# Optimization experiments

Hardware: AMD Instinct MI355X
Metric: run time of the kernel (lower is better)

Reference implementation:

```python
import jax, jax.numpy as jnp
import numpy as np

BN_EPS = 1e-5


def setup_inputs() -> dict:
    key = jax.random.key(0)
    k1, k2, k3, k4 = jax.random.split(key, 4)
    B, H, W, C = 2, 256, 256, 256
    x = jax.random.normal(k1, (B, H, W, C), dtype=jnp.float32)
    # 1x1 conv weights (bias=False), randomly initialized each forward in the original
    w_down = jax.random.normal(k2, (16, C), dtype=jnp.float32) * (1.0 / np.sqrt(C))
    w_up = jax.random.normal(k3, (C, 16), dtype=jnp.float32) * (1.0 / np.sqrt(16))
    w_final = jax.random.normal(k4, (C, 2 * C), dtype=jnp.float32) * (1.0 / np.sqrt(2 * C))
    return {"x": x, "w_down": w_down, "w_up": w_up, "w_final": w_final}


def reference(x, w_down, w_up, w_final):
    # x: [B, H, W, C] -> NCHW
    x = jnp.transpose(x, (0, 3, 1, 2))  # [B, C, H, W]
    B, C, H, W = x.shape
    # fresh BatchNorm2d in training mode: batch stats, weight=1, bias=0
    mean = jnp.mean(x, axis=(0, 2, 3), keepdims=True)
    var = jnp.var(x, axis=(0, 2, 3), keepdims=True)  # biased variance
    xn = (x - mean) * jax.lax.rsqrt(var + BN_EPS)  # [B, C, H, W]
    # relu -> sigmoid
    a = jax.nn.sigmoid(jax.nn.relu(xn))
    # down-channel 1x1 conv: C -> 16
    y = jnp.einsum('oc,bchw->bohw', w_down, a)  # [B, 16, H, W]
    f = y.reshape(B, 16, H * W)  # flattened per-sample [16, HW]
    # channel self-attention; NOTE: source bug reuses Gram of sample 0 for sample 1
    G0 = f[0] @ f[0].T  # [16, 16]
    out0 = G0 @ f[0]    # [16, HW]
    out1 = G0 @ f[1]    # [16, HW]  (faithful to xcam4b = Dot(xcam3a, xcam1b))
    xcam4 = jnp.stack([out0, out1], axis=0).reshape(B, 16, H, W)
    # up-channel 1x1 conv: 16 -> C
    up = jnp.einsum('co,bohw->bchw', w_up, xcam4)  # [B, C, H, W]
    cat = jnp.concatenate([xn, up], axis=1)  # [B, 2C, H, W]
    # final down-channel 1x1 conv: 2C -> C
    out = jnp.einsum('oc,bchw->bohw', w_final, cat)  # [B, C, H, W]
    return out
```

## Files before the change

kernel.cpp:

```cpp
#include <hip/hip_runtime.h>
#include <stdint.h>

typedef __attribute__((ext_vector_type(8))) short bf16x8;
typedef __attribute__((ext_vector_type(4))) float f32x4;

#define CC 256
#define HWP 65536

__device__ __forceinline__ unsigned short f2bf(float f) {
    union { float f; unsigned int u; } v; v.f = f;
    unsigned int u = v.u;
    return (unsigned short)((u + 0x7fffu + ((u >> 16) & 1u)) >> 16);
}
__device__ __forceinline__ unsigned int f2bf2(float lo, float hi) {
    return (unsigned)f2bf(lo) | ((unsigned)f2bf(hi) << 16);
}
__device__ __forceinline__ float sigm_relu(float xn) {
    float xr = fmaxf(xn, 0.f);
    float e = __expf(-xr);
    return __builtin_amdgcn_rcpf(1.f + e);
}

__global__ __launch_bounds__(512, 8) void k1_part(const float* __restrict__ x,
                                                  float* __restrict__ part) {
    __shared__ float red[8][520];
    const int t = threadIdx.x, bid = blockIdx.x;
    const int c4 = (t & 63) * 4, po = t >> 6;
    const float* xp = x + ((size_t)(bid * 256 + po)) * CC + c4;
    f32x4 s = {0.f, 0.f, 0.f, 0.f}, q = {0.f, 0.f, 0.f, 0.f};
    #pragma unroll 8
    for (int p = 0; p < 32; ++p) {
        f32x4 v = *(const f32x4*)(xp + (size_t)p * 8 * CC);
        s += v; q += v * v;
    }
    *(f32x4*)&red[po][c4] = s;
    *(f32x4*)&red[po][256 + c4] = q;
    __syncthreads();
    float r = 0.f;
    #pragma unroll
    for (int po2 = 0; po2 < 8; ++po2) r += red[po2][t];
    part[bid * 512 + t] = r;
}

__global__ __launch_bounds__(256) void k2a_red(const float* __restrict__ part,
                                               float* __restrict__ p2) {
    int t = threadIdx.x, r = blockIdx.x;
    float s = 0.f, q = 0.f;
    #pragma unroll
    for (int i = 0; i < 16; ++i) {
        s += part[(size_t)(r * 16 + i) * 512 + t];
        q += part[(size_t)(r * 16 + i) * 512 + 256 + t];
    }
    p2[r * 512 + t] = s;
    p2[r * 512 + 256 + t] = q;
}

__global__ __launch_bounds__(256) void k2b_stats(const float* __restrict__ p2,
                                                 float* __restrict__ mg,
                                                 float* __restrict__ ig) {
    int c = threadIdx.x;
    float s = 0.f, q = 0.f;
    #pragma unroll
    for (int r = 0; r < 32; ++r) { s += p2[r * 512 + c]; q += p2[r * 512 + 256 + c]; }
    float mean = s * (1.f / 131072.f);
    float var  = q * (1.f / 131072.f) - mean * mean;
    mg[c] = mean;
    ig[c] = rsqrtf(var + 1e-5f);
}

__global__ __launch_bounds__(512) void k3_gram(const float* __restrict__ x,
                                               const float* __restrict__ wd,
                                               const float* __restrict__ mg,
                                               const float* __restrict__ ig,
                                               float* __restrict__ gpart) {
    __shared__ uint4 apack[2048];
    __shared__ float y_s[2][16][68];
    const int t = threadIdx.x;
    const int w = t >> 6, lm = t & 15, lk = (t >> 4) & 3;
    const int h = w & 1, ntile = w >> 1;
    uint4 wfrag[4];
    #pragma unroll
    for (int kt = 0; kt < 4; ++kt) {
        const int kbr = h * 16 + kt * 4 + lk;
        f32x4 wa = *(const f32x4*)(wd + lm * 256 + kbr * 8);
        f32x4 wb = *(const f32x4*)(wd + lm * 256 + kbr * 8 + 4);
        wfrag[kt] = (uint4){f2bf2(wa[0], wa[1]), f2bf2(wa[2], wa[3]),
                            f2bf2(wb[0], wb[1]), f2bf2(wb[2], wb[3])};
    }
    const int kb = t & 31, c0 = kb * 8, nb = t >> 5;
    f32x4 m0 = *(const f32x4*)(mg + c0), m1 = *(const f32x4*)(mg + c0 + 4);
    f32x4 i0 = *(const f32x4*)(ig + c0), i1 = *(const f32x4*)(ig + c0 + 4);
    const float mm[8] = {m0[0],m0[1],m0[2],m0[3],m1[0],m1[1],m1[2],m1[3]};
    const float ii[8] = {i0[0],i0[1],i0[2],i0[3],i1[0],i1[1],i1[2],i1[3]};
    const int o1 = t >> 4, o2 = t & 15;
    float g = 0.f;
    for (int st = 0; st < 4; ++st) {
        const float* xb = x + ((size_t)(blockIdx.x * 256 + st * 64 + nb)) * CC + c0;
        #pragma unroll
        for (int rep = 0; rep < 4; ++rep) {
            int n = rep * 16 + nb;
            const float* xp = xb + (size_t)rep * 16 * CC;
            f32x4 v0 = *(const f32x4*)xp;
            f32x4 v1 = *(const f32x4*)(xp + 4);
            float vv[8] = {v0[0],v0[1],v0[2],v0[3],v1[0],v1[1],v1[2],v1[3]};
            unsigned aw[4];
            #pragma unroll
            for (int hh = 0; hh < 4; ++hh) {
                float a0 = sigm_relu((vv[2*hh]   - mm[2*hh])   * ii[2*hh]);
                float a1 = sigm_relu((vv[2*hh+1] - mm[2*hh+1]) * ii[2*hh+1]);
                aw[hh] = f2bf2(a0, a1);
            }
            apack[kb * 64 + (n ^ kb)] = (uint4){aw[0], aw[1], aw[2], aw[3]};
        }
        __syncthreads();
        f32x4 accY = {0.f, 0.f, 0.f, 0.f};
        #pragma unroll
        for (int kt = 0; kt < 4; ++kt) {
            const int kbr = h * 16 + kt * 4 + lk;
            uint4 u = apack[kbr * 64 + ((ntile * 16 + lm) ^ kbr)];
            accY = __builtin_amdgcn_mfma_f32_16x16x32_bf16(*(bf16x8*)&wfrag[kt], *(bf16x8*)&u, accY, 0, 0, 0);
        }
        #pragma unroll
        for (int i = 0; i < 4; ++i) y_s[h][lk * 4 + i][ntile * 16 + lm] = accY[i];
        __syncthreads();
        if (t < 256) {
            #pragma unroll
            for (int p4 = 0; p4 < 16; ++p4) {
                f32x4 a0 = *(const f32x4*)&y_s[0][o1][p4 * 4];
                f32x4 a1 = *(const f32x4*)&y_s[1][o1][p4 * 4];
                f32x4 b0 = *(const f32x4*)&y_s[0][o2][p4 * 4];
                f32x4 b1 = *(const f32x4*)&y_s[1][o2][p4 * 4];
                f32x4 ya = a0 + a1, yb = b0 + b1;
                g += ya[0]*yb[0] + ya[1]*yb[1] + ya[2]*yb[2] + ya[3]*yb[3];
            }
        }
        __syncthreads();
    }
    if (t < 256) gpart[blockIdx.x * 256 + t] = g;
}

__global__ __launch_bounds__(256) void k4_R(const float* __restrict__ gpart,
                                            const float* __restrict__ wd,
                                            float* __restrict__ Rg) {
    __shared__ float G_s[256];
    const int t = threadIdx.x;
    float g = 0.f;
    #pragma unroll 8
    for (int i = 0; i < 256; ++i) g += gpart[i * 256 + t];
    G_s[t] = g;
    __syncthreads();
    #pragma unroll
    for (int o = 0; o < 16; ++o) {
        float r = 0.f;
        #pragma unroll
        for (int o2 = 0; o2 < 16; ++o2) r += G_s[o * 16 + o2] * wd[o2 * 256 + t];
        Rg[o * 256 + t] = r;
    }
}

__global__ __launch_bounds__(256) void k5_wcb(const float* __restrict__ wf,
                                              const float* __restrict__ wu,
                                              const float* __restrict__ Rg,
                                              unsigned short* __restrict__ wcb) {
    __shared__ float M_s[16][17];
    const int t = threadIdx.x;
    const int lr = t >> 4, j = t & 15;
    const int r = blockIdx.x * 16 + lr;
    const float* wfr = wf + (size_t)r * 512;
    float m = 0.f;
    for (int c = 0; c < 256; ++c) m += wfr[256 + c] * wu[c * 16 + j];
    M_s[lr][j] = m;
    __syncthreads();
    float Ml[16];
    #pragma unroll
    for (int o = 0; o < 16; ++o) Ml[o] = M_s[lr][o];
    unsigned short* wrow = wcb + (size_t)r * 512;
    for (int i = 0; i < 16; ++i) {
        int c = j + 16 * i;
        wrow[c] = f2bf(wfr[c]);
        float kv = 0.f;
        #pragma unroll
        for (int o = 0; o < 16; ++o) kv += Ml[o] * Rg[o * 256 + c];
        wrow[256 + c] = f2bf(kv);
    }
}

__global__ __launch_bounds__(512, 4) void k6_main(const float* __restrict__ x,
                                                  const unsigned short* __restrict__ wcb,
                                                  const float* __restrict__ mg,
                                                  const float* __restrict__ ig,
                                                  float* __restrict__ out) {
    __shared__ __align__(16) char smem[69632];
    uint4* zpack = (uint4*)smem;
    float* T = (float*)smem;
    const int t = threadIdx.x;
    const int tile = blockIdx.x;
    const int b = tile >> 10;
    const int pw = (tile & 1023) * 64;
    {
        const int kb = t & 31, c0 = kb * 8, nb = t >> 5;
        f32x4 m0 = *(const f32x4*)(mg + c0), m1 = *(const f32x4*)(mg + c0 + 4);
        f32x4 i0 = *(const f32x4*)(ig + c0), i1 = *(const f32x4*)(ig + c0 + 4);
        float mm[8] = {m0[0],m0[1],m0[2],m0[3],m1[0],m1[1],m1[2],m1[3]};
        float ii[8] = {i0[0],i0[1],i0[2],i0[3],i1[0],i1[1],i1[2],i1[3]};
        const float* xb = x + ((size_t)(b * HWP + pw + nb)) * CC + c0;
        #pragma unroll
        for (int rep = 0; rep < 4; ++rep) {
            int n = rep * 16 + nb;
            const float* xp = xb + (size_t)rep * 16 * CC;
            f32x4 v0 = *(const f32x4*)xp;
            f32x4 v1 = *(const f32x4*)(xp + 4);
            float vv[8] = {v0[0],v0[1],v0[2],v0[3],v1[0],v1[1],v1[2],v1[3]};
            unsigned xw[4], aw[4];
            #pragma unroll
            for (int hh = 0; hh < 4; ++hh) {
                float xn0 = (vv[2*hh]   - mm[2*hh])   * ii[2*hh];
                float xn1 = (vv[2*hh+1] - mm[2*hh+1]) * ii[2*hh+1];
                xw[hh] = f2bf2(xn0, xn1);
                aw[hh] = f2bf2(sigm_relu(xn0), sigm_relu(xn1));
            }
            zpack[kb * 64 + (n ^ kb)] = (uint4){xw[0], xw[1], xw[2], xw[3]};
            zpack[(kb + 32) * 64 + (n ^ (kb + 32))] = (uint4){aw[0], aw[1], aw[2], aw[3]};
        }
    }
    __syncthreads();
    const int w = t >> 6, lm = t & 15, lk = (t >> 4) & 3;
    const unsigned short* wrow = wcb + (size_t)(w * 32 + lm) * 512 + lk * 8;
    f32x4 acc[4][2];
    #pragma unroll
    for (int mt = 0; mt < 4; ++mt)
        #pragma unroll
        for (int nt = 0; nt < 2; ++nt) acc[mt][nt] = (f32x4){0.f, 0.f, 0.f, 0.f};
    #pragma unroll 4
    for (int kt = 0; kt < 16; ++kt) {
        const int kbr = kt * 4 + lk;
        bf16x8 zfr[4], wfr[2];
        #pragma unroll
        for (int mt = 0; mt < 4; ++mt) {
            uint4 u = zpack[kbr * 64 + ((mt * 16 + lm) ^ kbr)];
            zfr[mt] = *(bf16x8*)&u;
        }
        #pragma unroll
        for (int nt = 0; nt < 2; ++nt)
            wfr[nt] = *(const bf16x8*)(wrow + (size_t)nt * 16 * 512 + kt * 32);
        #pragma unroll
        for (int mt = 0; mt < 4; ++mt)
            #pragma unroll
            for (int nt = 0; nt < 2; ++nt)
                acc[mt][nt] = __builtin_amdgcn_mfma_f32_16x16x32_bf16(zfr[mt], wfr[nt], acc[mt][nt], 0, 0, 0);
    }
    __syncthreads();
    #pragma unroll
    for (int nt = 0; nt < 2; ++nt) {
        const int ch = w * 32 + nt * 16 + lm;
        #pragma unroll
        for (int mt = 0; mt < 4; ++mt)
            *(f32x4*)&T[ch * 68 + mt * 16 + lk * 4] = acc[mt][nt];
    }
    __syncthreads();
    {
        const int row0 = t >> 4, pxq = t & 15;
        float* ob = out + (size_t)b * 256 * HWP + pw + pxq * 4;
        #pragma unroll
        for (int j = 0; j < 8; ++j) {
            const int row = j * 32 + row0;
            f32x4 v = *(const f32x4*)&T[row * 68 + pxq * 4];
            __builtin_nontemporal_store(v, (f32x4*)(ob + (size_t)row * HWP));
        }
    }
}

extern "C" void kernel_launch(void* const* d_in, const int* in_sizes, int n_in,
                              void* d_out, int out_size, void* d_ws, size_t ws_size,
                              hipStream_t stream) {
    const float* x  = (const float*)d_in[0];
    const float* wd = (const float*)d_in[1];
    const float* wu = (const float*)d_in[2];
    const float* wf = (const float*)d_in[3];
    float* out = (float*)d_out;
    char* ws = (char*)d_ws;
    unsigned short* wcb = (unsigned short*)ws;
    float* part  = (float*)(ws + 262144);
    float* p2    = (float*)(ws + 1310720);
    float* mg    = (float*)(ws + 1376256);
    float* ig    = (float*)(ws + 1377280);
    float* gpart = (float*)(ws + 1378304);
    float* Rg    = (float*)(ws + 1640448);

    k1_part <<<dim3(512),  dim3(512), 0, stream>>>(x, part);
    k2a_red <<<dim3(32),   dim3(256), 0, stream>>>(part, p2);
    k2b_stats<<<dim3(1),   dim3(256), 0, stream>>>(p2, mg, ig);
    k3_gram <<<dim3(256),  dim3(512), 0, stream>>>(x, wd, mg, ig, gpart);
    k4_R    <<<dim3(1),    dim3(256), 0, stream>>>(gpart, wd, Rg);
    k5_wcb  <<<dim3(16),   dim3(256), 0, stream>>>(wf, wu, Rg, wcb);
    k6_main <<<dim3(2048), dim3(512), 0, stream>>>(x, wcb, mg, ig, out);
}
```

Before: 175.8 us.

## Make k6_main persistent with register-prefetched tiles and direct MFMA output stores

The main GEMM kernel becomes a persistent-style kernel of 1024 threads, each block processing 8 pixel tiles. The next tile's input is prefetched into registers while the current tile runs its MFMAs. The shared-memory transpose of the output is dropped: each wave now owns 16 output channels and stores accumulators directly to global memory with nontemporal stores. The intent is to hide global load latency and cut LDS round trips, at the cost of fewer blocks (256), extra barriers, and narrower 64-byte output segments per row. Bf16 packing also switches to the library conversion routine.

```diff
diff --git a/kernel.cpp b/kernel.cpp
--- a/kernel.cpp
+++ b/kernel.cpp
@@ -1,5 +1,7 @@
 #include <hip/hip_runtime.h>
+#include <hip/hip_bf16.h>
 #include <stdint.h>
+#include <string.h>
 
 typedef __attribute__((ext_vector_type(8))) short bf16x8;
 typedef __attribute__((ext_vector_type(4))) float f32x4;
@@ -14,6 +16,12 @@
 }
 __device__ __forceinline__ unsigned int f2bf2(float lo, float hi) {
     return (unsigned)f2bf(lo) | ((unsigned)f2bf(hi) << 16);
+}
+__device__ __forceinline__ unsigned int pk2(float lo, float hi) {
+    union { __hip_bfloat16 b; unsigned short s; } ul, uh;
+    ul.b = __float2bfloat16(lo);
+    uh.b = __float2bfloat16(hi);
+    return (unsigned)ul.s | ((unsigned)uh.s << 16);
 }
 __device__ __forceinline__ float sigm_relu(float xn) {
     float xr = fmaxf(xn, 0.f);
@@ -185,89 +193,95 @@
     }
 }
 
-__global__ __launch_bounds__(512, 4) void k6_main(const float* __restrict__ x,
-                                                  const unsigned short* __restrict__ wcb,
-                                                  const float* __restrict__ mg,
-                                                  const float* __restrict__ ig,
-                                                  float* __restrict__ out) {
-    __shared__ __align__(16) char smem[69632];
-    uint4* zpack = (uint4*)smem;
-    float* T = (float*)smem;
+__global__ __launch_bounds__(1024, 4) void k6_main(const float* __restrict__ x,
+                                                   const unsigned short* __restrict__ wcb,
+                                                   const float* __restrict__ mg,
+                                                   const float* __restrict__ ig,
+                                                   float* __restrict__ out) {
+    __shared__ uint4 zpack[4096];
     const int t = threadIdx.x;
-    const int tile = blockIdx.x;
-    const int b = tile >> 10;
-    const int pw = (tile & 1023) * 64;
-    {
-        const int kb = t & 31, c0 = kb * 8, nb = t >> 5;
-        f32x4 m0 = *(const f32x4*)(mg + c0), m1 = *(const f32x4*)(mg + c0 + 4);
-        f32x4 i0 = *(const f32x4*)(ig + c0), i1 = *(const f32x4*)(ig + c0 + 4);
-        float mm[8] = {m0[0],m0[1],m0[2],m0[3],m1[0],m1[1],m1[2],m1[3]};
-        float ii[8] = {i0[0],i0[1],i0[2],i0[3],i1[0],i1[1],i1[2],i1[3]};
-        const float* xb = x + ((size_t)(b * HWP + pw + nb)) * CC + c0;
-        #pragma unroll
-        for (int rep = 0; rep < 4; ++rep) {
-            int n = rep * 16 + nb;
-            const float* xp = xb + (size_t)rep * 16 * CC;
-            f32x4 v0 = *(const f32x4*)xp;
-            f32x4 v1 = *(const f32x4*)(xp + 4);
-            float vv[8] = {v0[0],v0[1],v0[2],v0[3],v1[0],v1[1],v1[2],v1[3]};
-            unsigned xw[4], aw[4];
-            #pragma unroll
-            for (int hh = 0; hh < 4; ++hh) {
-                float xn0 = (vv[2*hh]   - mm[2*hh])   * ii[2*hh];
-                float xn1 = (vv[2*hh+1] - mm[2*hh+1]) * ii[2*hh+1];
-                xw[hh] = f2bf2(xn0, xn1);
-                aw[hh] = f2bf2(sigm_relu(xn0), sigm_relu(xn1));
-            }
-            zpack[kb * 64 + (n ^ kb)] = (uint4){xw[0], xw[1], xw[2], xw[3]};
-            zpack[(kb + 32) * 64 + (n ^ (kb + 32))] = (uint4){aw[0], aw[1], aw[2], aw[3]};
-        }
-    }
-    __syncthreads();
+    const int kb = t & 31, c0 = kb * 8, nb = t >> 5;
     const int w = t >> 6, lm = t & 15, lk = (t >> 4) & 3;
-    const unsigned short* wrow = wcb + (size_t)(w * 32 + lm) * 512 + lk * 8;
-    f32x4 acc[4][2];
-    #pragma unroll
-    for (int mt = 0; mt < 4; ++mt)
-        #pragma unroll
-        for (int nt = 0; nt < 2; ++nt) acc[mt][nt] = (f32x4){0.f, 0.f, 0.f, 0.f};
-    #pragma unroll 4
-    for (int kt = 0; kt < 16; ++kt) {
-        const int kbr = kt * 4 + lk;
-        bf16x8 zfr[4], wfr[2];
-        #pragma unroll
-        for (int mt = 0; mt < 4; ++mt) {
-            uint4 u = zpack[kbr * 64 + ((mt * 16 + lm) ^ kbr)];
-            zfr[mt] = *(bf16x8*)&u;
-        }
-        #pragma unroll
-        for (int nt = 0; nt < 2; ++nt)
-            wfr[nt] = *(const bf16x8*)(wrow + (size_t)nt * 16 * 512 + kt * 32);
-        #pragma unroll
-        for (int mt = 0; mt < 4; ++mt)
-            #pragma unroll
-            for (int nt = 0; nt < 2; ++nt)
-                acc[mt][nt] = __builtin_amdgcn_mfma_f32_16x16x32_bf16(zfr[mt], wfr[nt], acc[mt][nt], 0, 0, 0);
-    }
-    __syncthreads();
-    #pragma unroll
-    for (int nt = 0; nt < 2; ++nt) {
-        const int ch = w * 32 + nt * 16 + lm;
-        #pragma unroll
-        for (int mt = 0; mt < 4; ++mt)
-            *(f32x4*)&T[ch * 68 + mt * 16 + lk * 4] = acc[mt][nt];
-    }
-    __syncthreads();
-    {
-        const int row0 = t >> 4, pxq = t & 15;
-        float* ob = out + (size_t)b * 256 * HWP + pw + pxq * 4;
-        #pragma unroll
-        for (int j = 0; j < 8; ++j) {
-            const int row = j * 32 + row0;
-            f32x4 v = *(const f32x4*)&T[row * 68 + pxq * 4];
-            __builtin_nontemporal_store(v, (f32x4*)(ob + (size_t)row * HWP));
-        }
-    }
+    const f32x4 m0 = *(const f32x4*)(mg + c0), m1 = *(const f32x4*)(mg + c0 + 4);
+    const f32x4 i0 = *(const f32x4*)(ig + c0), i1 = *(const f32x4*)(ig + c0 + 4);
+    const unsigned short* wrow = wcb + (size_t)(w * 16 + lm) * 512 + lk * 8;
+    const int T0 = blockIdx.x * 8;
+    f32x4 rA[4], rB[4];
+
+#define LOADT(R, TI) do { \
+        const int b_ = (TI) >> 10, pw_ = ((TI) & 1023) * 64; \
+        const float* xb_ = x + ((size_t)(b_ * HWP + pw_ + nb)) * CC + c0; \
+        R[0] = *(const f32x4*)xb_;            R[1] = *(const f32x4*)(xb_ + 4); \
+        R[2] = *(const f32x4*)(xb_ + 32*CC);  R[3] = *(const f32x4*)(xb_ + 32*CC + 4); \
+    } while (0)
+
+#define CONVT(R) do { \
+        _Pragma("unroll") \
+        for (int rep = 0; rep < 2; ++rep) { \
+            const int n_ = rep * 32 + nb; \
+            f32x4 v0 = R[rep*2], v1 = R[rep*2+1]; \
+            float vv[8] = {v0[0],v0[1],v0[2],v0[3],v1[0],v1[1],v1[2],v1[3]}; \
+            float mmv[8] = {m0[0],m0[1],m0[2],m0[3],m1[0],m1[1],m1[2],m1[3]}; \
+            float iiv[8] = {i0[0],i0[1],i0[2],i0[3],i1[0],i1[1],i1[2],i1[3]}; \
+            unsigned xw[4], aw[4]; \
+            _Pragma("unroll") \
+            for (int hh = 0; hh < 4; ++hh) { \
+                float xn0 = (vv[2*hh]   - mmv[2*hh])   * iiv[2*hh]; \
+                float xn1 = (vv[2*hh+1] - mmv[2*hh+1]) * iiv[2*hh+1]; \
+                xw[hh] = pk2(xn0, xn1); \
+                aw[hh] = pk2(sigm_relu(xn0), sigm_relu(xn1)); \
+            } \
+            zpack[kb * 64 + (n_ ^ kb)] = (uint4){xw[0], xw[1], xw[2], xw[3]}; \
+            zpack[(kb + 32) * 64 + (n_ ^ (kb + 32))] = (uint4){aw[0], aw[1], aw[2], aw[3]}; \
+        } \
+    } while (0)
+
+#define MFMAST(TI) do { \
+        f32x4 acc_[4]; \
+        _Pragma("unroll") \
+        for (int mt = 0; mt < 4; ++mt) acc_[mt] = (f32x4){0.f, 0.f, 0.f, 0.f}; \
+        _Pragma("unroll") \
+        for (int kt = 0; kt < 16; ++kt) { \
+            const int kbr_ = kt * 4 + lk; \
+            bf16x8 wfr_ = *(const bf16x8*)(wrow + kt * 32); \
+            _Pragma("unroll") \
+            for (int mt = 0; mt < 4; ++mt) { \
+                uint4 u_ = zpack[kbr_ * 64 + ((mt * 16 + lm) ^ kbr_)]; \
+                acc_[mt] = __builtin_amdgcn_mfma_f32_16x16x32_bf16(*(bf16x8*)&u_, wfr_, acc_[mt], 0, 0, 0); \
+            } \
+        } \
+        const int b_ = (TI) >> 10, pw_ = ((TI) & 1023) * 64; \
+        float* ob_ = out + ((size_t)(b_ * 256 + w * 16 + lm)) * HWP + pw_ + lk * 4; \
+        _Pragma("unroll") \
+        for (int mt = 0; mt < 4; ++mt) \
+            __builtin_nontemporal_store(acc_[mt], (f32x4*)(ob_ + mt * 16)); \
+    } while (0)
+
+    LOADT(rA, T0);
+    CONVT(rA);
+    LOADT(rB, T0 + 1);
+    __syncthreads();
+    #pragma unroll 1
+    for (int i = 0; i < 3; ++i) {
+        MFMAST(T0 + 2 * i);
+        __syncthreads();
+        CONVT(rB);
+        LOADT(rA, T0 + 2 * i + 2);
+        __syncthreads();
+        MFMAST(T0 + 2 * i + 1);
+        __syncthreads();
+        CONVT(rA);
+        LOADT(rB, T0 + 2 * i + 3);
+        __syncthreads();
+    }
+    MFMAST(T0 + 6);
+    __syncthreads();
+    CONVT(rB);
+    __syncthreads();
+    MFMAST(T0 + 7);
+#undef LOADT
+#undef CONVT
+#undef MFMAST
 }
 
 extern "C" void kernel_launch(void* const* d_in, const int* in_sizes, int n_in,
@@ -287,11 +301,11 @@
     float* gpart = (float*)(ws + 1378304);
     float* Rg    = (float*)(ws + 1640448);
 
-    k1_part <<<dim3(512),  dim3(512), 0, stream>>>(x, part);
-    k2a_red <<<dim3(32),   dim3(256), 0, stream>>>(part, p2);
-    k2b_stats<<<dim3(1),   dim3(256), 0, stream>>>(p2, mg, ig);
-    k3_gram <<<dim3(256),  dim3(512), 0, stream>>>(x, wd, mg, ig, gpart);
-    k4_R    <<<dim3(1),    dim3(256), 0, stream>>>(gpart, wd, Rg);
-    k5_wcb  <<<dim3(16),   dim3(256), 0, stream>>>(wf, wu, Rg, wcb);
-    k6_main <<<dim3(2048), dim3(512), 0, stream>>>(x, wcb, mg, ig, out);
-}
+    k1_part <<<dim3(512),  dim3(512),  0, stream>>>(x, part);
+    k2a_red <<<dim3(32),   dim3(256),  0, stream>>>(part, p2);
+    k2b_stats<<<dim3(1),   dim3(256),  0, stream>>>(p2, mg, ig);
+    k3_gram <<<dim3(256),  dim3(512),  0, stream>>>(x, wd, mg, ig, gpart);
+    k4_R    <<<dim3(1),    dim3(256),  0, stream>>>(gpart, wd, Rg);
+    k5_wcb  <<<dim3(16),   dim3(256),  0, stream>>>(wf, wu, Rg, wcb);
+    k6_main <<<dim3(256),  dim3(1024), 0, stream>>>(x, wcb, mg, ig, out);
+}
```

Measured after the change: 294.9 us. +67.8%, slower.

## Halve k6 pixel tile, drop LDS transpose staging, write accumulators directly

Applied to the files above, without the earlier changes.

The main fused GEMM kernel now processes 32 pixels per block instead of 64, doubling the grid and shrinking LDS to 32 KB so that more blocks can be resident (launch bounds raised to 8). The LDS transpose buffer for the output and its two barriers are removed, and MFMA accumulators are stored straight to global memory as 16-byte nontemporal stores. Block indices are remapped in a strided order, and the hand-written bf16 rounding is replaced by the HIP intrinsic. The tradeoff is that each block reloads the weight fragments for only half as many pixels, and the direct output stores are less coalesced (64-byte runs per channel row).

```diff
diff --git a/kernel.cpp b/kernel.cpp
--- a/kernel.cpp
+++ b/kernel.cpp
@@ -1,4 +1,5 @@
 #include <hip/hip_runtime.h>
+#include <hip/hip_bf16.h>
 #include <stdint.h>
 
 typedef __attribute__((ext_vector_type(8))) short bf16x8;
@@ -12,8 +13,11 @@
     unsigned int u = v.u;
     return (unsigned short)((u + 0x7fffu + ((u >> 16) & 1u)) >> 16);
 }
-__device__ __forceinline__ unsigned int f2bf2(float lo, float hi) {
-    return (unsigned)f2bf(lo) | ((unsigned)f2bf(hi) << 16);
+__device__ __forceinline__ unsigned int pk2(float lo, float hi) {
+    union { __hip_bfloat16 b; unsigned short s; } ul, uh;
+    ul.b = __float2bfloat16(lo);
+    uh.b = __float2bfloat16(hi);
+    return (unsigned)ul.s | ((unsigned)uh.s << 16);
 }
 __device__ __forceinline__ float sigm_relu(float xn) {
     float xr = fmaxf(xn, 0.f);
@@ -84,8 +88,8 @@
         const int kbr = h * 16 + kt * 4 + lk;
         f32x4 wa = *(const f32x4*)(wd + lm * 256 + kbr * 8);
         f32x4 wb = *(const f32x4*)(wd + lm * 256 + kbr * 8 + 4);
-        wfrag[kt] = (uint4){f2bf2(wa[0], wa[1]), f2bf2(wa[2], wa[3]),
-                            f2bf2(wb[0], wb[1]), f2bf2(wb[2], wb[3])};
+        wfrag[kt] = (uint4){pk2(wa[0], wa[1]), pk2(wa[2], wa[3]),
+                            pk2(wb[0], wb[1]), pk2(wb[2], wb[3])};
     }
     const int kb = t & 31, c0 = kb * 8, nb = t >> 5;
     f32x4 m0 = *(const f32x4*)(mg + c0), m1 = *(const f32x4*)(mg + c0 + 4);
@@ -108,7 +112,7 @@
             for (int hh = 0; hh < 4; ++hh) {
                 float a0 = sigm_relu((vv[2*hh]   - mm[2*hh])   * ii[2*hh]);
                 float a1 = sigm_relu((vv[2*hh+1] - mm[2*hh+1]) * ii[2*hh+1]);
-                aw[hh] = f2bf2(a0, a1);
+                aw[hh] = pk2(a0, a1);
             }
             apack[kb * 64 + (n ^ kb)] = (uint4){aw[0], aw[1], aw[2], aw[3]};
         }
@@ -185,88 +189,77 @@
     }
 }
 
-__global__ __launch_bounds__(512, 4) void k6_main(const float* __restrict__ x,
+__global__ __launch_bounds__(512, 8) void k6_main(const float* __restrict__ x,
                                                   const unsigned short* __restrict__ wcb,
                                                   const float* __restrict__ mg,
                                                   const float* __restrict__ ig,
                                                   float* __restrict__ out) {
-    __shared__ __align__(16) char smem[69632];
-    uint4* zpack = (uint4*)smem;
-    float* T = (float*)smem;
-    const int t = threadIdx.x;
-    const int tile = blockIdx.x;
-    const int b = tile >> 10;
-    const int pw = (tile & 1023) * 64;
+    __shared__ uint4 zpack[2048];
+    const int t = threadIdx.x;
+    const int tile = (blockIdx.x & 7) * 512 + (blockIdx.x >> 3);
+    const int b = tile >> 11;
+    const int pw = (tile & 2047) * 32;
     {
-        const int kb = t & 31, c0 = kb * 8, nb = t >> 5;
+        const int px = t >> 4, ci = t & 15, c0 = ci * 16;
         f32x4 m0 = *(const f32x4*)(mg + c0), m1 = *(const f32x4*)(mg + c0 + 4);
+        f32x4 m2 = *(const f32x4*)(mg + c0 + 8), m3 = *(const f32x4*)(mg + c0 + 12);
         f32x4 i0 = *(const f32x4*)(ig + c0), i1 = *(const f32x4*)(ig + c0 + 4);
-        float mm[8] = {m0[0],m0[1],m0[2],m0[3],m1[0],m1[1],m1[2],m1[3]};
-        float ii[8] = {i0[0],i0[1],i0[2],i0[3],i1[0],i1[1],i1[2],i1[3]};
-        const float* xb = x + ((size_t)(b * HWP + pw + nb)) * CC + c0;
-        #pragma unroll
-        for (int rep = 0; rep < 4; ++rep) {
-            int n = rep * 16 + nb;
-            const float* xp = xb + (size_t)rep * 16 * CC;
-            f32x4 v0 = *(const f32x4*)xp;
-            f32x4 v1 = *(const f32x4*)(xp + 4);
-            float vv[8] = {v0[0],v0[1],v0[2],v0[3],v1[0],v1[1],v1[2],v1[3]};
-            unsigned xw[4], aw[4];
-            #pragma unroll
-            for (int hh = 0; hh < 4; ++hh) {
-                float xn0 = (vv[2*hh]   - mm[2*hh])   * ii[2*hh];
-                float xn1 = (vv[2*hh+1] - mm[2*hh+1]) * ii[2*hh+1];
-                xw[hh] = f2bf2(xn0, xn1);
-                aw[hh] = f2bf2(sigm_relu(xn0), sigm_relu(xn1));
-            }
-            zpack[kb * 64 + (n ^ kb)] = (uint4){xw[0], xw[1], xw[2], xw[3]};
-            zpack[(kb + 32) * 64 + (n ^ (kb + 32))] = (uint4){aw[0], aw[1], aw[2], aw[3]};
-        }
+        f32x4 i2 = *(const f32x4*)(ig + c0 + 8), i3 = *(const f32x4*)(ig + c0 + 12);
+        const float* xp = x + ((size_t)(b * HWP + pw + px)) * CC + c0;
+        f32x4 v0 = *(const f32x4*)xp,       v1 = *(const f32x4*)(xp + 4);
+        f32x4 v2 = *(const f32x4*)(xp + 8), v3 = *(const f32x4*)(xp + 12);
+        float vv[16] = {v0[0],v0[1],v0[2],v0[3],v1[0],v1[1],v1[2],v1[3],
+                        v2[0],v2[1],v2[2],v2[3],v3[0],v3[1],v3[2],v3[3]};
+        float mm[16] = {m0[0],m0[1],m0[2],m0[3],m1[0],m1[1],m1[2],m1[3],
+                        m2[0],m2[1],m2[2],m2[3],m3[0],m3[1],m3[2],m3[3]};
+        float ii[16] = {i0[0],i0[1],i0[2],i0[3],i1[0],i1[1],i1[2],i1[3],
+                        i2[0],i2[1],i2[2],i2[3],i3[0],i3[1],i3[2],i3[3]};
+        unsigned xw[8], aw[8];
+        #pragma unroll
+        for (int hh = 0; hh < 8; ++hh) {
+            float xn0 = (vv[2*hh]   - mm[2*hh])   * ii[2*hh];
+            float xn1 = (vv[2*hh+1] - mm[2*hh+1]) * ii[2*hh+1];
+            xw[hh] = pk2(xn0, xn1);
+            aw[hh] = pk2(sigm_relu(xn0), sigm_relu(xn1));
+        }
+        const int kb0 = ci * 2;
+        zpack[kb0 * 32 + ((px ^ kb0) & 31)]              = (uint4){xw[0], xw[1], xw[2], xw[3]};
+        zpack[(kb0+1) * 32 + ((px ^ (kb0+1)) & 31)]      = (uint4){xw[4], xw[5], xw[6], xw[7]};
+        zpack[(kb0+32) * 32 + ((px ^ (kb0+32)) & 31)]    = (uint4){aw[0], aw[1], aw[2], aw[3]};
+        zpack[(kb0+33) * 32 + ((px ^ (kb0+33)) & 31)]    = (uint4){aw[4], aw[5], aw[6], aw[7]};
     }
     __syncthreads();
     const int w = t >> 6, lm = t & 15, lk = (t >> 4) & 3;
     const unsigned short* wrow = wcb + (size_t)(w * 32 + lm) * 512 + lk * 8;
-    f32x4 acc[4][2];
-    #pragma unroll
-    for (int mt = 0; mt < 4; ++mt)
+    f32x4 acc[2][2];
+    #pragma unroll
+    for (int mt = 0; mt < 2; ++mt)
         #pragma unroll
         for (int nt = 0; nt < 2; ++nt) acc[mt][nt] = (f32x4){0.f, 0.f, 0.f, 0.f};
     #pragma unroll 4
     for (int kt = 0; kt < 16; ++kt) {
         const int kbr = kt * 4 + lk;
-        bf16x8 zfr[4], wfr[2];
-        #pragma unroll
-        for (int mt = 0; mt < 4; ++mt) {
-            uint4 u = zpack[kbr * 64 + ((mt * 16 + lm) ^ kbr)];
+        bf16x8 zfr[2], wfr[2];
+        #pragma unroll
+        for (int mt = 0; mt < 2; ++mt) {
+            uint4 u = zpack[kbr * 32 + (((mt * 16 + lm) ^ kbr) & 31)];
             zfr[mt] = *(bf16x8*)&u;
         }
         #pragma unroll
         for (int nt = 0; nt < 2; ++nt)
             wfr[nt] = *(const bf16x8*)(wrow + (size_t)nt * 16 * 512 + kt * 32);
         #pragma unroll
-        for (int mt = 0; mt < 4; ++mt)
+        for (int mt = 0; mt < 2; ++mt)
             #pragma unroll
             for (int nt = 0; nt < 2; ++nt)
                 acc[mt][nt] = __builtin_amdgcn_mfma_f32_16x16x32_bf16(zfr[mt], wfr[nt], acc[mt][nt], 0, 0, 0);
     }
-    __syncthreads();
     #pragma unroll
     for (int nt = 0; nt < 2; ++nt) {
-        const int ch = w * 32 + nt * 16 + lm;
-        #pragma unroll
-        for (int mt = 0; mt < 4; ++mt)
-            *(f32x4*)&T[ch * 68 + mt * 16 + lk * 4] = acc[mt][nt];
-    }
-    __syncthreads();
-    {
-        const int row0 = t >> 4, pxq = t & 15;
-        float* ob = out + (size_t)b * 256 * HWP + pw + pxq * 4;
-        #pragma unroll
-        for (int j = 0; j < 8; ++j) {
-            const int row = j * 32 + row0;
-            f32x4 v = *(const f32x4*)&T[row * 68 + pxq * 4];
-            __builtin_nontemporal_store(v, (f32x4*)(ob + (size_t)row * HWP));
-        }
+        float* ob = out + ((size_t)(b * 256 + w * 32 + nt * 16 + lm)) * HWP + pw + lk * 4;
+        #pragma unroll
+        for (int mt = 0; mt < 2; ++mt)
+            __builtin_nontemporal_store(acc[mt][nt], (f32x4*)(ob + mt * 16));
     }
 }
 
@@ -293,5 +286,5 @@
     k3_gram <<<dim3(256),  dim3(512), 0, stream>>>(x, wd, mg, ig, gpart);
     k4_R    <<<dim3(1),    dim3(256), 0, stream>>>(gpart, wd, Rg);
     k5_wcb  <<<dim3(16),   dim3(256), 0, stream>>>(wf, wu, Rg, wcb);
-    k6_main <<<dim3(2048), dim3(512), 0, stream>>>(x, wcb, mg, ig, out);
-}
+    k6_main <<<dim3(4096), dim3(512), 0, stream>>>(x, wcb, mg, ig, out);
+}
```

Result: slower. 241.6 us (+37.4%).
